# Optimization experiments

Measured on AMD Instinct MI355X. Metric: run time of the kernel, lower is better.

Reference implementation:

```python
import jax, jax.numpy as jnp
import numpy as np
from jax import lax

C = 192       # filter_channels
L = 3         # n_layers
K = 3         # kernel_size
NB = 10       # num_bins
TB = 5.0      # tail_bound
HALF = 1      # in_channels // 2


def setup_inputs() -> dict:
    key = jax.random.key(0)
    ks = jax.random.split(key, 8)
    s = lambda i, shape: jax.random.normal(ks[i], shape, jnp.float32) * 0.05
    return {
        "x": jax.random.normal(ks[0], (16, 2, 8192), jnp.float32),
        "x_mask": jnp.ones((16, 1, 8192), jnp.float32),
        "w_pre": s(1, (C, HALF)), "b_pre": jnp.zeros((C,), jnp.float32),
        "sep_w": s(2, (L, K, 1, C)), "sep_b": jnp.zeros((L, C), jnp.float32),
        "pw_w": s(3, (L, C, C)), "pw_b": jnp.zeros((L, C), jnp.float32),
        "n1_g": jnp.ones((L, C), jnp.float32), "n1_b": jnp.zeros((L, C), jnp.float32),
        "n2_g": jnp.ones((L, C), jnp.float32), "n2_b": jnp.zeros((L, C), jnp.float32),
        "w_proj": s(4, (HALF * (3 * NB - 1), C)),
        "b_proj": jnp.zeros((HALF * (3 * NB - 1),), jnp.float32),
    }


def _layernorm_c(x, g, b, eps=1e-5):
    # normalize over channel axis (axis=1) of [b, c, t]
    m = jnp.mean(x, axis=1, keepdims=True)
    v = jnp.var(x, axis=1, keepdims=True)
    return (x - m) * lax.rsqrt(v + eps) * g[:, None] + b[:, None]


def _rq_spline(x, uw, uh, ud, tail_bound=TB, mw=1e-3, mh=1e-3, md=1e-3):
    """Unconstrained rational-quadratic spline with linear tails (forward)."""
    nb = uw.shape[-1]
    inside = (x >= -tail_bound) & (x <= tail_bound)
    const = float(np.log(np.exp(1.0 - md) - 1.0))
    ud = jnp.pad(ud, [(0, 0)] * (ud.ndim - 1) + [(1, 1)], constant_values=const)

    widths = jax.nn.softmax(uw, axis=-1)
    widths = mw + (1.0 - mw * nb) * widths
    cw = jnp.pad(jnp.cumsum(widths, -1), [(0, 0)] * (widths.ndim - 1) + [(1, 0)])
    cw = -tail_bound + 2.0 * tail_bound * cw
    cw = cw.at[..., 0].set(-tail_bound).at[..., -1].set(tail_bound)
    w = cw[..., 1:] - cw[..., :-1]

    heights = jax.nn.softmax(uh, axis=-1)
    heights = mh + (1.0 - mh * nb) * heights
    ch = jnp.pad(jnp.cumsum(heights, -1), [(0, 0)] * (heights.ndim - 1) + [(1, 0)])
    ch = -tail_bound + 2.0 * tail_bound * ch
    ch = ch.at[..., 0].set(-tail_bound).at[..., -1].set(tail_bound)
    hgt = ch[..., 1:] - ch[..., :-1]

    d = md + jax.nn.softplus(ud)  # [..., nb+1]

    xi = jnp.clip(x, -tail_bound, tail_bound)
    # searchsorted-style bin lookup
    idx = jnp.clip(jnp.sum((xi[..., None] >= cw).astype(jnp.int32), -1) - 1, 0, nb - 1)
    take = lambda p: jnp.take_along_axis(p, idx[..., None], axis=-1)[..., 0]

    in_cw, in_w = take(cw), take(w)
    in_ch, in_h = take(ch), take(hgt)
    in_d, d_p = take(d), take(d[..., 1:])
    delta = in_h / in_w

    th = (xi - in_cw) / in_w
    th1 = th * (1.0 - th)
    num = in_h * (delta * th * th + in_d * th1)
    den = delta + (in_d + d_p - 2.0 * delta) * th1
    y = in_ch + num / den
    dnum = delta * delta * (d_p * th * th + 2.0 * delta * th1 + in_d * (1.0 - th) ** 2)
    lad = jnp.log(dnum) - 2.0 * jnp.log(den)

    y = jnp.where(inside, y, x)
    lad = jnp.where(inside, lad, jnp.zeros_like(lad))
    return y, lad


def reference(x, x_mask, w_pre, b_pre, sep_w, sep_b, pw_w, pw_b,
              n1_g, n1_b, n2_g, n2_b, w_proj, b_proj):
    x0, x1 = x[:, :HALF], x[:, HALF:]

    # pre: 1x1 conv
    h = jnp.einsum('bct,fc->bft', x0, w_pre) + b_pre[:, None]

    # DDSConv: depthwise dilated conv + 1x1 + LayerNorm + GELU, residual
    for i in range(L):
        y = lax.conv_general_dilated(
            h * x_mask, sep_w[i], window_strides=(1,), padding='SAME',
            rhs_dilation=(K ** i,),
            dimension_numbers=('NCH', 'HIO', 'NCH'),
            feature_group_count=C) + sep_b[i][:, None]
        y = jax.nn.gelu(_layernorm_c(y, n1_g[i], n1_b[i]), approximate=False)
        y = jnp.einsum('bct,oc->bot', y, pw_w[i]) + pw_b[i][:, None]
        y = jax.nn.gelu(_layernorm_c(y, n2_g[i], n2_b[i]), approximate=False)
        h = h + y
    h = h * x_mask

    # proj: 1x1 conv to spline params
    h = (jnp.einsum('bct,oc->bot', h, w_proj) + b_proj[:, None]) * x_mask

    b, c, t = x0.shape
    h = h.reshape(b, c, 3 * NB - 1, t).transpose(0, 1, 3, 2)  # [b, c, t, 3*NB-1]
    scale = 1.0 / np.sqrt(C).astype(np.float32)
    uw = h[..., :NB] * scale
    uh = h[..., NB:2 * NB] * scale
    ud = h[..., 2 * NB:]

    y1, lad = _rq_spline(x1, uw, uh, ud)
    out = jnp.concatenate([x0, y1], axis=1) * x_mask
    logdet = jnp.sum(lad * x_mask, axis=(1, 2))
    return out, logdet
```

## Files before the change

### kernel.cpp

```cpp
#include <hip/hip_runtime.h>

#define CC    192
#define EXT   64
#define LDC   216
#define NTH   512
#define NW    8
#define HALO  13
#define INTR  38
#define TT    8192
#define BATCH 16
#define NTILES 216
#define NPROJ 29

#define WQ1_ELEMS (3*6*12*512)
#define WQ2_ELEMS (6*2*512)

typedef __bf16 bf16x8 __attribute__((ext_vector_type(8)));
typedef __bf16 bf16x4 __attribute__((ext_vector_type(4)));
typedef float  f32x4  __attribute__((ext_vector_type(4)));

__device__ __forceinline__ float gelu_fast(float v) {
    float vv = v * v;
    float u2 = v * fmaf(0.0713548162f, vv, 1.5957691216f);
    float t  = __expf(u2);
    float r  = __builtin_amdgcn_rcpf(t + 1.0f);
    return v - v * r;
}
__device__ __forceinline__ float softplus_f(float v) {
    float e = __expf(-fabsf(v));
    return fmaxf(v, 0.0f) + __logf(1.0f + e);
}

__global__ __launch_bounds__(256) void prepack_kernel(
    const float* __restrict__ pw_w, const float* __restrict__ w_proj,
    __bf16* __restrict__ wq, __bf16* __restrict__ wq2) {
    int idx = blockIdx.x * 256 + threadIdx.x;
    if (idx < WQ1_ELEMS) {
        int e    = idx & 7;
        int lane = (idx >> 3) & 63;
        int r    = idx >> 9;
        int mt   = r % 12;
        int ks   = (r / 12) % 6;
        int li   = r / 72;
        int o = 16 * mt + (lane & 15);
        int c = 32 * ks + 8 * (lane >> 4) + e;
        wq[idx] = (__bf16)pw_w[((size_t)li * CC + o) * CC + c];
    } else if (idx < WQ1_ELEMS + WQ2_ELEMS) {
        int i2   = idx - WQ1_ELEMS;
        int e    = i2 & 7;
        int lane = (i2 >> 3) & 63;
        int r    = i2 >> 9;
        int pr   = r % 2;
        int ks   = r / 2;
        int row  = 16 * pr + (lane & 15);
        int c    = 32 * ks + 8 * (lane >> 4) + e;
        wq2[i2] = (row < NPROJ) ? (__bf16)w_proj[(size_t)row * CC + c] : (__bf16)0.0f;
    }
}

__global__ __launch_bounds__(NTH, 4) void convflow_kernel(
    const float* __restrict__ x, const float* __restrict__ xmask,
    const float* __restrict__ w_pre, const float* __restrict__ b_pre,
    const float* __restrict__ sep_w, const float* __restrict__ sep_b,
    const __bf16* __restrict__ wq, const __bf16* __restrict__ wq2,
    const float* __restrict__ pw_b,
    const float* __restrict__ n1_g, const float* __restrict__ n1_b,
    const float* __restrict__ n2_g, const float* __restrict__ n2_b,
    const float* __restrict__ b_proj,
    float* __restrict__ out, float* __restrict__ logdet)
{
    extern __shared__ char smemraw[];
    __bf16* __restrict__ sh_t = (__bf16*)smemraw;
    __bf16* __restrict__ syt  = sh_t + EXT * LDC;
    float*  __restrict__ sproj = (float*)syt;
    float*  __restrict__ fbase = (float*)(syt + EXT * LDC);
    float*  __restrict__ spb = fbase;
    float*  __restrict__ sg2 = fbase + 192;
    float*  __restrict__ sb2 = fbase + 384;
    float*  __restrict__ sx0 = fbase + 576;
    float*  __restrict__ sx1 = fbase + 640;
    float*  __restrict__ smk = fbase + 704;
    float2* __restrict__ sred = (float2*)(fbase + 768);

    const int tid  = threadIdx.x;
    const int lane = tid & 63;
    const int wav  = tid >> 6;
    const int b    = blockIdx.x / NTILES;
    const int tile = blockIdx.x - b * NTILES;
    const int t0   = tile * INTR - HALO;

    for (int j = tid; j < EXT; j += NTH) {
        int t = t0 + j;
        bool ok = (t >= 0) && (t < TT);
        sx0[j] = ok ? x[b*2*TT + t]      : 0.0f;
        sx1[j] = ok ? x[b*2*TT + TT + t] : 0.0f;
        smk[j] = ok ? xmask[b*TT + t]    : 0.0f;
    }
    __syncthreads();

    for (int e = tid; e < CC*EXT; e += NTH) {
        int c = e % CC;
        int j = e / CC;
        sh_t[j*LDC + c] = (__bf16)(sx0[j] * w_pre[c] + b_pre[c]);
    }
    for (int q = tid; q < INTR; q += NTH) {
        int t = t0 + HALO + q;
        if (t < TT) out[b*2*TT + t] = sx0[HALO+q] * smk[HALO+q];
    }
    __syncthreads();

    const int g   = lane >> 4;
    const int c15 = lane & 15;
    const int cl  = lane & 31;
    const int sub = lane >> 5;
    const int nt   = wav & 3;
    const int half = wav >> 2;

    #pragma unroll
    for (int li = 0; li < 3; ++li) {
        constexpr int DILA[3] = {1, 3, 9};
        constexpr int JLOA[3] = {1, 4, 13};
        constexpr int JHIA[3] = {63, 60, 51};
        const int dil = DILA[li];
        const int jlo = JLOA[li], jhi = JHIA[li];

        for (int i = tid; i < CC; i += NTH) {
            spb[i] = pw_b[li*CC + i];
            sg2[i] = n2_g[li*CC + i];
            sb2[i] = n2_b[li*CC + i];
        }

        {
            float k0[6], k1[6], k2[6], cb[6], g1[6], b1[6];
            #pragma unroll
            for (int k = 0; k < 6; ++k) {
                int c = cl + 32*k;
                k0[k] = sep_w[(li*3+0)*CC + c];
                k1[k] = sep_w[(li*3+1)*CC + c];
                k2[k] = sep_w[(li*3+2)*CC + c];
                cb[k] = sep_b[li*CC + c];
                g1[k] = n1_g[li*CC + c];
                b1[k] = n1_b[li*CC + c];
            }
            for (int j = jlo + 2*wav + sub; j < jhi; j += 16) {
                float m0 = smk[j-dil], m1 = smk[j], m2 = smk[j+dil];
                const __bf16* r0 = sh_t + (j-dil)*LDC;
                const __bf16* r1 = sh_t + j*LDC;
                const __bf16* r2 = sh_t + (j+dil)*LDC;
                float a[6]; float s = 0.0f, ss = 0.0f;
                #pragma unroll
                for (int k = 0; k < 6; ++k) {
                    int c = cl + 32*k;
                    float v = k0[k]*(float)r0[c]*m0 + k1[k]*(float)r1[c]*m1
                            + k2[k]*(float)r2[c]*m2 + cb[k];
                    a[k] = v; s += v; ss += v*v;
                }
                #pragma unroll
                for (int mm = 1; mm < 32; mm <<= 1) {
                    s  += __shfl_xor(s,  mm, 64);
                    ss += __shfl_xor(ss, mm, 64);
                }
                float mean = s * (1.0f/CC);
                float var  = ss * (1.0f/CC) - mean*mean;
                float rstd = rsqrtf(var + 1e-5f);
                #pragma unroll
                for (int k = 0; k < 6; ++k)
                    syt[j*LDC + cl + 32*k] = (__bf16)gelu_fast((a[k]-mean)*rstd*g1[k] + b1[k]);
            }
        }
        __syncthreads();

        {
            f32x4 acc[6];
            #pragma unroll
            for (int q = 0; q < 6; ++q) {
                float4 pb = *(const float4*)(spb + 16*(6*half+q) + 4*g);
                acc[q][0] = pb.x; acc[q][1] = pb.y; acc[q][2] = pb.z; acc[q][3] = pb.w;
            }
            const __bf16* wql = wq + (size_t)li * (6*12*512);
            #pragma unroll
            for (int ks = 0; ks < 6; ++ks) {
                bf16x8 bfrag = *(const bf16x8*)(syt + (16*nt + c15)*LDC + 32*ks + 8*g);
                const __bf16* ap = wql + (size_t)(ks*12 + 6*half)*512 + lane*8;
                #pragma unroll
                for (int q = 0; q < 6; ++q) {
                    bf16x8 afrag = *(const bf16x8*)(ap + (size_t)q*512);
                    acc[q] = __builtin_amdgcn_mfma_f32_16x16x32_bf16(afrag, bfrag, acc[q], 0, 0, 0);
                }
            }
            float s = 0.0f, ss = 0.0f;
            #pragma unroll
            for (int q = 0; q < 6; ++q) {
                #pragma unroll
                for (int e = 0; e < 4; ++e) { float z = acc[q][e]; s += z; ss += z*z; }
            }
            s  += __shfl_xor(s, 16, 64);  s  += __shfl_xor(s, 32, 64);
            ss += __shfl_xor(ss, 16, 64); ss += __shfl_xor(ss, 32, 64);
            if (lane < 16) sred[(16*nt + lane)*2 + half] = make_float2(s, ss);
            __syncthreads();
            const int col = 16*nt + c15;
            float2 e0 = sred[col*2], e1 = sred[col*2+1];
            float mean = (e0.x + e1.x) * (1.0f/CC);
            float var  = (e0.y + e1.y) * (1.0f/CC) - mean*mean;
            float rstd = rsqrtf(var + 1e-5f);
            #pragma unroll
            for (int q = 0; q < 6; ++q) {
                int mt = 6*half + q;
                float4 gv = *(const float4*)(sg2 + 16*mt + 4*g);
                float4 bv = *(const float4*)(sb2 + 16*mt + 4*g);
                bf16x4 hv = *(bf16x4*)(sh_t + (size_t)col*LDC + 16*mt + 4*g);
                hv[0] = (__bf16)((float)hv[0] + gelu_fast((acc[q][0]-mean)*rstd*gv.x + bv.x));
                hv[1] = (__bf16)((float)hv[1] + gelu_fast((acc[q][1]-mean)*rstd*gv.y + bv.y));
                hv[2] = (__bf16)((float)hv[2] + gelu_fast((acc[q][2]-mean)*rstd*gv.z + bv.z));
                hv[3] = (__bf16)((float)hv[3] + gelu_fast((acc[q][3]-mean)*rstd*gv.w + bv.w));
                *(bf16x4*)(sh_t + (size_t)col*LDC + 16*mt + 4*g) = hv;
            }
        }
        __syncthreads();
    }

    {
        const int pr = half;
        f32x4 p0 = {0,0,0,0};
        #pragma unroll
        for (int ks = 0; ks < 6; ++ks) {
            bf16x8 bfrag = *(const bf16x8*)(sh_t + (16*nt + c15)*LDC + 32*ks + 8*g);
            bf16x8 a0 = *(const bf16x8*)(wq2 + (size_t)(ks*2 + pr)*512 + lane*8);
            p0 = __builtin_amdgcn_mfma_f32_16x16x32_bf16(a0, bfrag, p0, 0, 0, 0);
        }
        const int col = 16*nt + c15;
        if (col >= HALO && col < HALO + INTR) {
            float mj = smk[col];
            #pragma unroll
            for (int e = 0; e < 4; ++e) {
                int p = 16*pr + 4*g + e;
                if (p < NPROJ) sproj[col*33 + p] = (p0[e]*mj + b_proj[p])*mj;
            }
        }
    }
    __syncthreads();

    if (tid < 64) {
        int j = HALO + tid;
        int t = t0 + j;
        float ladm = 0.0f;
        if (tid < INTR && t < TT) {
            const float SCALE = 0.07216878364870323f;
            float mj = smk[j];
            float uw[10], uh[10];
            #pragma unroll
            for (int k = 0; k < 10; ++k) {
                uw[k] = sproj[j*33 + k]      * SCALE;
                uh[k] = sproj[j*33 + 10 + k] * SCALE;
            }
            float mxw = uw[0];
            #pragma unroll
            for (int k = 1; k < 10; ++k) mxw = fmaxf(mxw, uw[k]);
            float ew[10]; float sew = 0.0f;
            #pragma unroll
            for (int k = 0; k < 10; ++k) { ew[k] = __expf(uw[k]-mxw); sew += ew[k]; }
            float invw = 1.0f/sew;
            float cw[11]; cw[0] = -5.0f;
            float run = 0.0f;
            #pragma unroll
            for (int k = 0; k < 10; ++k) { run += 0.001f + 0.99f*ew[k]*invw; cw[k+1] = -5.0f + 10.0f*run; }
            cw[10] = 5.0f;
            float mxh = uh[0];
            #pragma unroll
            for (int k = 1; k < 10; ++k) mxh = fmaxf(mxh, uh[k]);
            float eh[10]; float seh = 0.0f;
            #pragma unroll
            for (int k = 0; k < 10; ++k) { eh[k] = __expf(uh[k]-mxh); seh += eh[k]; }
            float invh = 1.0f/seh;
            float ch[11]; ch[0] = -5.0f;
            run = 0.0f;
            #pragma unroll
            for (int k = 0; k < 10; ++k) { run += 0.001f + 0.99f*eh[k]*invh; ch[k+1] = -5.0f + 10.0f*run; }
            ch[10] = 5.0f;
            float dd[11];
            dd[0] = 1.0f;
            #pragma unroll
            for (int k = 0; k < 9; ++k) dd[k+1] = 0.001f + softplus_f(sproj[j*33 + 20 + k]);
            dd[10] = 1.0f;

            float xv = sx1[j];
            bool inside = (xv >= -5.0f) && (xv <= 5.0f);
            float xi = fminf(fmaxf(xv, -5.0f), 5.0f);
            int idx = 0;
            #pragma unroll
            for (int k = 1; k <= 9; ++k) idx = (xi >= cw[k]) ? k : idx;
            float in_cw=0, in_w=1, in_ch=0, in_h=1, in_d=1, d_p=1;
            #pragma unroll
            for (int k = 0; k < 10; ++k) {
                if (k == idx) {
                    in_cw = cw[k]; in_w = cw[k+1]-cw[k];
                    in_ch = ch[k]; in_h = ch[k+1]-ch[k];
                    in_d  = dd[k]; d_p  = dd[k+1];
                }
            }
            float delta = in_h/in_w;
            float th  = (xi - in_cw)/in_w;
            float th1 = th*(1.0f-th);
            float num = in_h*(delta*th*th + in_d*th1);
            float den = delta + (in_d + d_p - 2.0f*delta)*th1;
            float yv  = in_ch + num/den;
            float omt = 1.0f - th;
            float dnum = delta*delta*(d_p*th*th + 2.0f*delta*th1 + in_d*omt*omt);
            float lad = __logf(dnum) - 2.0f*__logf(den);
            if (!inside) { yv = xv; lad = 0.0f; }
            out[b*2*TT + TT + t] = yv*mj;
            ladm = lad*mj;
        }
        #pragma unroll
        for (int mm = 1; mm < 64; mm <<= 1) ladm += __shfl_xor(ladm, mm, 64);
        if (tid == 0) atomicAdd(&logdet[b], ladm);
    }
}

extern "C" void kernel_launch(void* const* d_in, const int* in_sizes, int n_in,
                              void* d_out, int out_size, void* d_ws, size_t ws_size,
                              hipStream_t stream) {
    const float* x      = (const float*)d_in[0];
    const float* xmask  = (const float*)d_in[1];
    const float* w_pre  = (const float*)d_in[2];
    const float* b_pre  = (const float*)d_in[3];
    const float* sep_w  = (const float*)d_in[4];
    const float* sep_b  = (const float*)d_in[5];
    const float* pw_w   = (const float*)d_in[6];
    const float* pw_b   = (const float*)d_in[7];
    const float* n1_g   = (const float*)d_in[8];
    const float* n1_b   = (const float*)d_in[9];
    const float* n2_g   = (const float*)d_in[10];
    const float* n2_b   = (const float*)d_in[11];
    const float* w_proj = (const float*)d_in[12];
    const float* b_proj = (const float*)d_in[13];
    float* out = (float*)d_out;
    float* logdet = out + (size_t)BATCH*2*TT;
    __bf16* wq  = (__bf16*)d_ws;
    __bf16* wq2 = wq + WQ1_ELEMS;

    hipMemsetAsync((void*)logdet, 0, BATCH*sizeof(float), stream);
    prepack_kernel<<<dim3((WQ1_ELEMS + WQ2_ELEMS + 255)/256), 256, 0, stream>>>(
        pw_w, w_proj, wq, wq2);

    size_t shbytes = (size_t)(2*EXT*LDC*2 + 768*4 + 64*2*8);
    dim3 grid(BATCH*NTILES);
    convflow_kernel<<<grid, NTH, shbytes, stream>>>(
        x, xmask, w_pre, b_pre, sep_w, sep_b, wq, wq2, pw_b,
        n1_g, n1_b, n2_g, n2_b, b_proj, out, logdet);
}
```

Before: 255.4 us.

## Shrink shared memory, raise occupancy target, and fold mask into residual stream

Shrinks the LDS row pitch and drops the per-layer LDS staging of pw_b/n2 params in favour of direct global reads, cutting shared memory per block. Also raises launch bounds to 6 blocks per CU. The depthwise conv now uses a contiguous 6-channel-per-lane mapping with packed bf16x2 loads and stores. The mask is applied once when h is written rather than on every conv tap. The padding change alters LDS bank-conflict patterns for the MFMA fragment loads, and the tighter register budget at 6 blocks per CU could cause spills.

Result: slower. 272.0 us (+6.5%).

```diff
diff --git a/kernel.cpp b/kernel.cpp
--- a/kernel.cpp
+++ b/kernel.cpp
@@ -2,9 +2,8 @@
 
 #define CC    192
 #define EXT   64
-#define LDC   216
+#define LDC   200
 #define NTH   512
-#define NW    8
 #define HALO  13
 #define INTR  38
 #define TT    8192
@@ -17,6 +16,7 @@
 
 typedef __bf16 bf16x8 __attribute__((ext_vector_type(8)));
 typedef __bf16 bf16x4 __attribute__((ext_vector_type(4)));
+typedef __bf16 bf16x2 __attribute__((ext_vector_type(2)));
 typedef float  f32x4  __attribute__((ext_vector_type(4)));
 
 __device__ __forceinline__ float gelu_fast(float v) {
@@ -58,7 +58,7 @@
     }
 }
 
-__global__ __launch_bounds__(NTH, 4) void convflow_kernel(
+__global__ __launch_bounds__(NTH, 6) void convflow_kernel(
     const float* __restrict__ x, const float* __restrict__ xmask,
     const float* __restrict__ w_pre, const float* __restrict__ b_pre,
     const float* __restrict__ sep_w, const float* __restrict__ sep_b,
@@ -74,13 +74,10 @@
     __bf16* __restrict__ syt  = sh_t + EXT * LDC;
     float*  __restrict__ sproj = (float*)syt;
     float*  __restrict__ fbase = (float*)(syt + EXT * LDC);
-    float*  __restrict__ spb = fbase;
-    float*  __restrict__ sg2 = fbase + 192;
-    float*  __restrict__ sb2 = fbase + 384;
-    float*  __restrict__ sx0 = fbase + 576;
-    float*  __restrict__ sx1 = fbase + 640;
-    float*  __restrict__ smk = fbase + 704;
-    float2* __restrict__ sred = (float2*)(fbase + 768);
+    float*  __restrict__ sx0 = fbase;
+    float*  __restrict__ sx1 = fbase + 64;
+    float*  __restrict__ smk = fbase + 128;
+    float2* __restrict__ sred = (float2*)(fbase + 192);
 
     const int tid  = threadIdx.x;
     const int lane = tid & 63;
@@ -101,7 +98,7 @@
     for (int e = tid; e < CC*EXT; e += NTH) {
         int c = e % CC;
         int j = e / CC;
-        sh_t[j*LDC + c] = (__bf16)(sx0[j] * w_pre[c] + b_pre[c]);
+        sh_t[j*LDC + c] = (__bf16)((sx0[j] * w_pre[c] + b_pre[c]) * smk[j]);
     }
     for (int q = tid; q < INTR; q += NTH) {
         int t = t0 + HALO + q;
@@ -124,17 +121,11 @@
         const int dil = DILA[li];
         const int jlo = JLOA[li], jhi = JHIA[li];
 
-        for (int i = tid; i < CC; i += NTH) {
-            spb[i] = pw_b[li*CC + i];
-            sg2[i] = n2_g[li*CC + i];
-            sb2[i] = n2_b[li*CC + i];
-        }
-
         {
             float k0[6], k1[6], k2[6], cb[6], g1[6], b1[6];
             #pragma unroll
             for (int k = 0; k < 6; ++k) {
-                int c = cl + 32*k;
+                int c = 6*cl + k;
                 k0[k] = sep_w[(li*3+0)*CC + c];
                 k1[k] = sep_w[(li*3+1)*CC + c];
                 k2[k] = sep_w[(li*3+2)*CC + c];
@@ -143,16 +134,18 @@
                 b1[k] = n1_b[li*CC + c];
             }
             for (int j = jlo + 2*wav + sub; j < jhi; j += 16) {
-                float m0 = smk[j-dil], m1 = smk[j], m2 = smk[j+dil];
-                const __bf16* r0 = sh_t + (j-dil)*LDC;
-                const __bf16* r1 = sh_t + j*LDC;
-                const __bf16* r2 = sh_t + (j+dil)*LDC;
+                const bf16x2* r0 = (const bf16x2*)(sh_t + (j-dil)*LDC + 6*cl);
+                const bf16x2* r1 = (const bf16x2*)(sh_t + j*LDC       + 6*cl);
+                const bf16x2* r2 = (const bf16x2*)(sh_t + (j+dil)*LDC + 6*cl);
+                bf16x2 t0v[3], t1v[3], t2v[3];
+                #pragma unroll
+                for (int p = 0; p < 3; ++p) { t0v[p] = r0[p]; t1v[p] = r1[p]; t2v[p] = r2[p]; }
                 float a[6]; float s = 0.0f, ss = 0.0f;
                 #pragma unroll
                 for (int k = 0; k < 6; ++k) {
-                    int c = cl + 32*k;
-                    float v = k0[k]*(float)r0[c]*m0 + k1[k]*(float)r1[c]*m1
-                            + k2[k]*(float)r2[c]*m2 + cb[k];
+                    float v = k0[k]*(float)t0v[k>>1][k&1]
+                            + k1[k]*(float)t1v[k>>1][k&1]
+                            + k2[k]*(float)t2v[k>>1][k&1] + cb[k];
                     a[k] = v; s += v; ss += v*v;
                 }
                 #pragma unroll
@@ -164,17 +157,22 @@
                 float var  = ss * (1.0f/CC) - mean*mean;
                 float rstd = rsqrtf(var + 1e-5f);
                 #pragma unroll
-                for (int k = 0; k < 6; ++k)
-                    syt[j*LDC + cl + 32*k] = (__bf16)gelu_fast((a[k]-mean)*rstd*g1[k] + b1[k]);
+                for (int p = 0; p < 3; ++p) {
+                    bf16x2 w;
+                    w[0] = (__bf16)gelu_fast((a[2*p+0]-mean)*rstd*g1[2*p+0] + b1[2*p+0]);
+                    w[1] = (__bf16)gelu_fast((a[2*p+1]-mean)*rstd*g1[2*p+1] + b1[2*p+1]);
+                    *(bf16x2*)(syt + j*LDC + 6*cl + 2*p) = w;
+                }
             }
         }
         __syncthreads();
 
         {
+            const float* pwbl = pw_b + li*CC;
             f32x4 acc[6];
             #pragma unroll
             for (int q = 0; q < 6; ++q) {
-                float4 pb = *(const float4*)(spb + 16*(6*half+q) + 4*g);
+                float4 pb = *(const float4*)(pwbl + 16*(6*half+q) + 4*g);
                 acc[q][0] = pb.x; acc[q][1] = pb.y; acc[q][2] = pb.z; acc[q][3] = pb.w;
             }
             const __bf16* wql = wq + (size_t)li * (6*12*512);
@@ -203,16 +201,19 @@
             float mean = (e0.x + e1.x) * (1.0f/CC);
             float var  = (e0.y + e1.y) * (1.0f/CC) - mean*mean;
             float rstd = rsqrtf(var + 1e-5f);
+            float mj   = smk[col];
+            const float* g2l = n2_g + li*CC;
+            const float* b2l = n2_b + li*CC;
             #pragma unroll
             for (int q = 0; q < 6; ++q) {
                 int mt = 6*half + q;
-                float4 gv = *(const float4*)(sg2 + 16*mt + 4*g);
-                float4 bv = *(const float4*)(sb2 + 16*mt + 4*g);
+                float4 gv = *(const float4*)(g2l + 16*mt + 4*g);
+                float4 bv = *(const float4*)(b2l + 16*mt + 4*g);
                 bf16x4 hv = *(bf16x4*)(sh_t + (size_t)col*LDC + 16*mt + 4*g);
-                hv[0] = (__bf16)((float)hv[0] + gelu_fast((acc[q][0]-mean)*rstd*gv.x + bv.x));
-                hv[1] = (__bf16)((float)hv[1] + gelu_fast((acc[q][1]-mean)*rstd*gv.y + bv.y));
-                hv[2] = (__bf16)((float)hv[2] + gelu_fast((acc[q][2]-mean)*rstd*gv.z + bv.z));
-                hv[3] = (__bf16)((float)hv[3] + gelu_fast((acc[q][3]-mean)*rstd*gv.w + bv.w));
+                hv[0] = (__bf16)((float)hv[0] + gelu_fast((acc[q][0]-mean)*rstd*gv.x + bv.x)*mj);
+                hv[1] = (__bf16)((float)hv[1] + gelu_fast((acc[q][1]-mean)*rstd*gv.y + bv.y)*mj);
+                hv[2] = (__bf16)((float)hv[2] + gelu_fast((acc[q][2]-mean)*rstd*gv.z + bv.z)*mj);
+                hv[3] = (__bf16)((float)hv[3] + gelu_fast((acc[q][3]-mean)*rstd*gv.w + bv.w)*mj);
                 *(bf16x4*)(sh_t + (size_t)col*LDC + 16*mt + 4*g) = hv;
             }
         }
@@ -234,7 +235,7 @@
             #pragma unroll
             for (int e = 0; e < 4; ++e) {
                 int p = 16*pr + 4*g + e;
-                if (p < NPROJ) sproj[col*33 + p] = (p0[e]*mj + b_proj[p])*mj;
+                if (p < NPROJ) sproj[col*33 + p] = (p0[e] + b_proj[p])*mj;
             }
         }
     }
@@ -343,7 +344,7 @@
     prepack_kernel<<<dim3((WQ1_ELEMS + WQ2_ELEMS + 255)/256), 256, 0, stream>>>(
         pw_w, w_proj, wq, wq2);
 
-    size_t shbytes = (size_t)(2*EXT*LDC*2 + 768*4 + 64*2*8);
+    size_t shbytes = (size_t)(2*EXT*LDC*2 + 192*4 + 64*2*8);
     dim3 grid(BATCH*NTILES);
     convflow_kernel<<<grid, NTH, shbytes, stream>>>(
         x, xmask, w_pre, b_pre, sep_w, sep_b, wq, wq2, pw_b,
```
